# Optimization experiments

Hardware: AMD Instinct MI355X
Metric: run time of the kernel (lower is better)

The kernel has to match this reference:

```python
import jax, jax.numpy as jnp
import numpy as np


def _grid_sample_bilinear_border(img, px, py):
    # img: [B,C,H,W]; px,py: [B,H,W] absolute pixel coords (align_corners=True)
    B, C, H, W = img.shape
    # border padding: clamp sample coords into valid range
    px = jnp.clip(px, 0.0, W - 1.0)
    py = jnp.clip(py, 0.0, H - 1.0)
    x0f = jnp.floor(px)
    y0f = jnp.floor(py)
    wx = px - x0f  # [B,H,W]
    wy = py - y0f
    x0 = jnp.clip(x0f.astype(jnp.int32), 0, W - 1)
    x1 = jnp.clip(x0 + 1, 0, W - 1)
    y0 = jnp.clip(y0f.astype(jnp.int32), 0, H - 1)
    y1 = jnp.clip(y0 + 1, 0, H - 1)

    flat = img.reshape(B, C, H * W)

    def gather(yi, xi):
        idx = (yi * W + xi).reshape(B, 1, H * W)
        return jnp.take_along_axis(flat, idx, axis=2).reshape(B, C, H, W)

    v00 = gather(y0, x0)
    v01 = gather(y0, x1)
    v10 = gather(y1, x0)
    v11 = gather(y1, x1)
    wx = wx[:, None]  # [B,1,H,W]
    wy = wy[:, None]
    top = v00 * (1.0 - wx) + v01 * wx
    bot = v10 * (1.0 - wx) + v11 * wx
    return top * (1.0 - wy) + bot * wy


def setup_inputs() -> dict:
    key = jax.random.key(0)
    k1, k2 = jax.random.split(key)
    B, C, H, W = 8, 64, 512, 512
    x = jax.random.normal(k1, (B, C, H, W), dtype=jnp.float32)
    flow = jax.random.normal(k2, (B, 2, H, W), dtype=jnp.float32)
    return {"x": x, "flow": flow}


def reference(x, flow):
    B, C, H, W = x.shape
    # Original builds a normalized grid then grid_sample unnormalizes it;
    # net effect: sample at absolute coords (gridX + u, gridY + v).
    gx = jnp.arange(W, dtype=x.dtype)[None, None, :]  # [1,1,W]
    gy = jnp.arange(H, dtype=x.dtype)[None, :, None]  # [1,H,1]
    px = gx + flow[:, 0]  # [B,H,W]
    py = gy + flow[:, 1]
    x_warp = _grid_sample_bilinear_border(x, px, py)
    return (x_warp, flow)
```

## Files before the change

kernel.cpp:

```cpp
#include <hip/hip_runtime.h>

#define BB 8
#define CC 64
#define HH 512
#define WW 512
#define CG 16
#define NCG (CC / CG)
#define NXCD 8

typedef float f4 __attribute__((ext_vector_type(4)));

__global__ __launch_bounds__(256) void align2d_warp_kernel(
    const float* __restrict__ x,
    const float* __restrict__ flow,
    float* __restrict__ out)
{
    const int nwg = BB * NCG * HH * 2;
    const int cpx = nwg / NXCD;
    const int bid = blockIdx.x;
    const int wg  = (bid % NXCD) * cpx + bid / NXCD;

    const int b     = wg / (NCG * HH * 2);
    int rem         = wg % (NCG * HH * 2);
    const int cg    = rem / (HH * 2);
    rem             = rem % (HH * 2);
    const int h     = rem >> 1;
    const int whalf = rem & 1;
    const int w     = whalf * 256 + threadIdx.x;

    const int pix = h * WW + w;
    const float fx = flow[((size_t)b * 2 + 0) * (HH * WW) + pix];
    const float fy = flow[((size_t)b * 2 + 1) * (HH * WW) + pix];

    float px = fminf(fmaxf((float)w + fx, 0.0f), (float)(WW - 1));
    float py = fminf(fmaxf((float)h + fy, 0.0f), (float)(HH - 1));
    float x0f = floorf(px);
    float y0f = floorf(py);
    float wx = px - x0f;
    float wy = py - y0f;
    int x0 = (int)x0f;
    int y0 = (int)y0f;
    int x1 = min(x0 + 1, WW - 1);
    int y1 = min(y0 + 1, HH - 1);

    const int o00 = y0 * WW + x0;
    const int o01 = y0 * WW + x1;
    const int o10 = y1 * WW + x0;
    const int o11 = y1 * WW + x1;

    const float w00 = (1.0f - wx) * (1.0f - wy);
    const float w01 = wx * (1.0f - wy);
    const float w10 = (1.0f - wx) * wy;
    const float w11 = wx * wy;

    const float* xb = x   + ((size_t)b * CC + (size_t)cg * CG) * (HH * WW);
    float*       ob = out + ((size_t)b * CC + (size_t)cg * CG) * (HH * WW) + pix;

    #pragma unroll 8
    for (int c = 0; c < CG; ++c) {
        const float* p = xb + (size_t)c * (HH * WW);
        float v = p[o00] * w00 + p[o01] * w01 + p[o10] * w10 + p[o11] * w11;
        __builtin_nontemporal_store(v, ob + (size_t)c * (HH * WW));
    }
}

__global__ __launch_bounds__(256) void align2d_flowcopy_kernel(
    const f4* __restrict__ flow, f4* __restrict__ out)
{
    const int i = blockIdx.x * blockDim.x + threadIdx.x;
    f4 v = __builtin_nontemporal_load(flow + i);
    __builtin_nontemporal_store(v, out + i);
}

extern "C" void kernel_launch(void* const* d_in, const int* in_sizes, int n_in,
                              void* d_out, int out_size, void* d_ws, size_t ws_size,
                              hipStream_t stream) {
    const float* x    = (const float*)d_in[0];
    const float* flow = (const float*)d_in[1];
    float* out = (float*)d_out;

    const int nwg = BB * NCG * HH * 2;
    align2d_warp_kernel<<<nwg, 256, 0, stream>>>(x, flow, out);

    const int nflow4 = (BB * 2 * HH * WW) / 4;
    float* out_flow = out + (size_t)BB * CC * HH * WW;
    align2d_flowcopy_kernel<<<nflow4 / 256, 256, 0, stream>>>(
        (const f4*)flow, (f4*)out_flow);
}
```

Measured before the change: 1.143 ms.

## Stage per-channel row band in LDS and gather bilinear taps from shared memory

The work split changes from one workgroup per row and channel group to one workgroup per channel and 8-row tile. Each workgroup copies a band of input rows (the tile plus a radius of 8) into LDS with vector loads, then serves the four bilinear taps from LDS, falling back to global memory when a sample lands outside the band. The aim is to replace scattered global gathers with coalesced bulk loads plus LDS reads. In exchange, the band overfetches about 25 rows per 8 output rows, flow is reread once per channel rather than once per 16 channels, and the roughly 50KB of LDS per workgroup limits occupancy.

```diff
diff --git a/kernel.cpp b/kernel.cpp
--- a/kernel.cpp
+++ b/kernel.cpp
@@ -4,8 +4,10 @@
 #define CC 64
 #define HH 512
 #define WW 512
-#define CG 16
-#define NCG (CC / CG)
+#define TH 8
+#define RAD 8
+#define SRMAX (TH + 2 * RAD + 1)
+#define NT (HH / TH)
 #define NXCD 8
 
 typedef float f4 __attribute__((ext_vector_type(4)));
@@ -15,52 +17,74 @@
     const float* __restrict__ flow,
     float* __restrict__ out)
 {
-    const int nwg = BB * NCG * HH * 2;
+    __shared__ float lds[SRMAX * WW];
+
+    const int nwg = BB * CC * NT;
     const int cpx = nwg / NXCD;
-    const int bid = blockIdx.x;
-    const int wg  = (bid % NXCD) * cpx + bid / NXCD;
+    const int wg  = (blockIdx.x % NXCD) * cpx + blockIdx.x / NXCD;
 
-    const int b     = wg / (NCG * HH * 2);
-    int rem         = wg % (NCG * HH * 2);
-    const int cg    = rem / (HH * 2);
-    rem             = rem % (HH * 2);
-    const int h     = rem >> 1;
-    const int whalf = rem & 1;
-    const int w     = whalf * 256 + threadIdx.x;
+    const int t = wg & (NT - 1);
+    const int c = (wg >> 6) & (CC - 1);
+    const int b = wg >> 12;
 
-    const int pix = h * WW + w;
-    const float fx = flow[((size_t)b * 2 + 0) * (HH * WW) + pix];
-    const float fy = flow[((size_t)b * 2 + 1) * (HH * WW) + pix];
+    const int h0   = t * TH;
+    const int W_lo = max(0, h0 - RAD);
+    const int W_hi = min(HH - 1, h0 + TH + RAD);
+    const int SR   = W_hi - W_lo + 1;
 
-    float px = fminf(fmaxf((float)w + fx, 0.0f), (float)(WW - 1));
-    float py = fminf(fmaxf((float)h + fy, 0.0f), (float)(HH - 1));
-    float x0f = floorf(px);
-    float y0f = floorf(py);
-    float wx = px - x0f;
-    float wy = py - y0f;
-    int x0 = (int)x0f;
-    int y0 = (int)y0f;
-    int x1 = min(x0 + 1, WW - 1);
-    int y1 = min(y0 + 1, HH - 1);
+    const float* xc = x + ((size_t)b * CC + c) * (HH * WW);
 
-    const int o00 = y0 * WW + x0;
-    const int o01 = y0 * WW + x1;
-    const int o10 = y1 * WW + x0;
-    const int o11 = y1 * WW + x1;
+    {
+        const f4* src = (const f4*)(xc + (size_t)W_lo * WW);
+        f4*       dst = (f4*)lds;
+        const int n4 = SR * (WW / 4);
+        for (int i = threadIdx.x; i < n4; i += 256) dst[i] = src[i];
+    }
+    __syncthreads();
 
-    const float w00 = (1.0f - wx) * (1.0f - wy);
-    const float w01 = wx * (1.0f - wy);
-    const float w10 = (1.0f - wx) * wy;
-    const float w11 = wx * wy;
+    const float* fpx = flow + ((size_t)b * 2 + 0) * (HH * WW);
+    const float* fpy = flow + ((size_t)b * 2 + 1) * (HH * WW);
+    float*       ob  = out + ((size_t)b * CC + c) * (HH * WW);
 
-    const float* xb = x   + ((size_t)b * CC + (size_t)cg * CG) * (HH * WW);
-    float*       ob = out + ((size_t)b * CC + (size_t)cg * CG) * (HH * WW) + pix;
+    #pragma unroll 4
+    for (int i = 0; i < (TH * WW) / 256; ++i) {
+        const int p   = i * 256 + threadIdx.x;
+        const int hh  = h0 + (p >> 9);
+        const int ww  = p & (WW - 1);
+        const int pix = hh * WW + ww;
 
-    #pragma unroll 8
-    for (int c = 0; c < CG; ++c) {
-        const float* p = xb + (size_t)c * (HH * WW);
-        float v = p[o00] * w00 + p[o01] * w01 + p[o10] * w10 + p[o11] * w11;
-        __builtin_nontemporal_store(v, ob + (size_t)c * (HH * WW));
+        const float fx = fpx[pix];
+        const float fy = fpy[pix];
+
+        float px = fminf(fmaxf((float)ww + fx, 0.0f), (float)(WW - 1));
+        float py = fminf(fmaxf((float)hh + fy, 0.0f), (float)(HH - 1));
+        float x0f = floorf(px);
+        float y0f = floorf(py);
+        float wx = px - x0f;
+        float wy = py - y0f;
+        int x0 = (int)x0f;
+        int y0 = (int)y0f;
+        int x1 = min(x0 + 1, WW - 1);
+        int y1 = min(y0 + 1, HH - 1);
+
+        float v00, v01, v10, v11;
+        if (y0 >= W_lo && y1 <= W_hi) {
+            const int r0 = (y0 - W_lo) * WW;
+            const int r1 = (y1 - W_lo) * WW;
+            v00 = lds[r0 + x0]; v01 = lds[r0 + x1];
+            v10 = lds[r1 + x0]; v11 = lds[r1 + x1];
+        } else {
+            v00 = xc[y0 * WW + x0]; v01 = xc[y0 * WW + x1];
+            v10 = xc[y1 * WW + x0]; v11 = xc[y1 * WW + x1];
+        }
+
+        const float w00 = (1.0f - wx) * (1.0f - wy);
+        const float w01 = wx * (1.0f - wy);
+        const float w10 = (1.0f - wx) * wy;
+        const float w11 = wx * wy;
+        float v = v00 * w00 + v01 * w01 + v10 * w10 + v11 * w11;
+
+        __builtin_nontemporal_store(v, ob + pix);
     }
 }
 
@@ -79,7 +103,7 @@
     const float* flow = (const float*)d_in[1];
     float* out = (float*)d_out;
 
-    const int nwg = BB * NCG * HH * 2;
+    const int nwg = BB * CC * NT;
     align2d_warp_kernel<<<nwg, 256, 0, stream>>>(x, flow, out);
 
     const int nflow4 = (BB * 2 * HH * WW) / 4;
```

Result: slower. 1.190 ms (+4.1%).
